# Performance work log

Measured on AMD Instinct MI355X. Metric: run time of the kernel, lower is better.

Reference implementation:

```python
import jax, jax.numpy as jnp
import numpy as np

MASK_RATIO = 0.02
N2V_W, WAV_W, TV_W = 1.0, 0.2, 0.01
THRESHOLD = 50.0
LEVELS = 3


def setup_inputs() -> dict:
    key = jax.random.key(0)
    k1, k2, k3 = jax.random.split(key, 3)
    shape = (64, 1, 512, 512)
    pred = jax.random.uniform(k1, shape, dtype=jnp.float32)
    noisy_input = jax.random.uniform(k2, shape, dtype=jnp.float32)
    # N2V random blind-spot mask (torch.rand_like(pred) < mask_ratio)
    mask = jax.random.uniform(k3, shape, dtype=jnp.float32) < MASK_RATIO
    return {"pred": pred, "noisy_input": noisy_input, "mask": mask}


def haar_dwt2(x):
    # x: [B, H, W] with H, W even. Single-level 2D Haar DWT (pywt 'haar').
    a = x[:, 0::2, 0::2]
    b = x[:, 0::2, 1::2]
    c = x[:, 1::2, 0::2]
    d = x[:, 1::2, 1::2]
    ll = (a + b + c + d) * 0.5
    ch = (a + b - c - d) * 0.5  # horizontal detail
    cv = (a - b + c - d) * 0.5  # vertical detail
    cd = (a - b - c + d) * 0.5  # diagonal detail
    return ll, ch, cv, cd


def _level_l1(c, thr):
    # L1 between coeff and its (detached) soft-thresholded version
    target = jax.lax.stop_gradient(jnp.sign(c) * jnp.maximum(jnp.abs(c) - thr, 0.0))
    return jnp.mean(jnp.abs(c - target))


def reference(pred, noisy_input, mask):
    p = jnp.clip(pred, 0.0, 1.0)

    # --- Noise2Void masked L1 ---
    m = mask.astype(p.dtype)
    n2v = jnp.sum(jnp.abs(p - noisy_input) * m) / jnp.maximum(jnp.sum(m), 1.0)

    # --- Wavelet sparsity (multi-level Haar, soft-threshold targets) ---
    x = p[:, 0]  # [B, H, W]
    details = []  # finest first
    for _ in range(LEVELS):
        x, ch, cv, cd = haar_dwt2(x)
        details.append((ch, cv, cd))
    wav = jnp.asarray(0.0, dtype=p.dtype)
    for level_idx in range(1, LEVELS + 1):  # level_idx=1 -> coarsest (wavedec2 order)
        ch, cv, cd = details[LEVELS - level_idx]
        thr = (THRESHOLD / (2.0 ** (level_idx - 1))) / 255.0
        lvl = (_level_l1(ch, thr) + _level_l1(cv, thr) + _level_l1(cd, thr)) / 3.0
        wav = wav + (1.0 / level_idx) * lvl

    # --- Total variation ---
    tv = jnp.mean(jnp.abs(p[:, :, 1:, :] - p[:, :, :-1, :])) + \
         jnp.mean(jnp.abs(p[:, :, :, 1:] - p[:, :, :, :-1]))

    return N2V_W * n2v + WAV_W * wav + TV_W * tv
```

## Files before the change

kernel.cpp:

```cpp
#include <hip/hip_runtime.h>

#define NIMG 64
#define H 512
#define W 512

constexpr float THR_64  = 50.0f / 255.0f;
constexpr float THR_128 = 50.0f / 2.0f / 255.0f;
constexpr float THR_256 = 50.0f / 4.0f / 255.0f;

__device__ __forceinline__ float wave_sum(float v) {
#pragma unroll
    for (int o = 32; o > 0; o >>= 1) v += __shfl_down(v, o, 64);
    return v;
}

__device__ __forceinline__ float clip01(float x) {
    return fminf(fmaxf(x, 0.0f), 1.0f);
}

__device__ __forceinline__ float4 clip4(float4 p) {
    p.x = clip01(p.x); p.y = clip01(p.y); p.z = clip01(p.z); p.w = clip01(p.w);
    return p;
}

__global__ __launch_bounds__(256) void kA(const float* __restrict__ pred,
                                          const float* __restrict__ noisy,
                                          const int* __restrict__ mask,
                                          float4* __restrict__ pA,
                                          float* __restrict__ pW2,
                                          float* __restrict__ ll2) {
    __shared__ float sl[9 * 512];
    __shared__ float red[4][5];

    const int tid = threadIdx.x;
    const int lane = tid & 63;
    const int wv = tid >> 6;
    const int bid = blockIdx.x;
    const int n = bid >> 6;
    const int s = bid & 63;
    const int r0 = s << 3;
    const size_t base = (size_t)n * (H * W) + (size_t)r0 * W;
    const size_t o0 = base + (size_t)tid * 4;

    float4 p0 = *reinterpret_cast<const float4*>(pred + o0);
    float4 p1 = *reinterpret_cast<const float4*>(pred + o0 + 1024);
    float4 p2 = *reinterpret_cast<const float4*>(pred + o0 + 2048);
    float4 p3 = *reinterpret_cast<const float4*>(pred + o0 + 3072);
    int4 m0 = *reinterpret_cast<const int4*>(mask + o0);
    int4 m1 = *reinterpret_cast<const int4*>(mask + o0 + 1024);
    int4 m2 = *reinterpret_cast<const int4*>(mask + o0 + 2048);
    int4 m3 = *reinterpret_cast<const int4*>(mask + o0 + 3072);
    if (tid < 128) {
        float4 hp = make_float4(0.f, 0.f, 0.f, 0.f);
        if (r0 > 0) {
            hp = clip4(*reinterpret_cast<const float4*>(pred + base - W + (size_t)tid * 4));
        }
        *reinterpret_cast<float4*>(&sl[(8 << 9) + (tid << 2)]) = hp;
    }

    float n2v = 0.0f, msum = 0.0f;
#define CHUNK(P, MK, OFS)                                                        \
    {                                                                            \
        float4 nz = make_float4(0.f, 0.f, 0.f, 0.f);                             \
        if ((MK.x | MK.y | MK.z | MK.w) != 0)                                    \
            nz = *reinterpret_cast<const float4*>(noisy + (OFS));                \
        P = clip4(P);                                                            \
        float m;                                                                 \
        m = MK.x ? 1.f : 0.f; n2v += fabsf(P.x - nz.x) * m; msum += m;           \
        m = MK.y ? 1.f : 0.f; n2v += fabsf(P.y - nz.y) * m; msum += m;           \
        m = MK.z ? 1.f : 0.f; n2v += fabsf(P.z - nz.z) * m; msum += m;           \
        m = MK.w ? 1.f : 0.f; n2v += fabsf(P.w - nz.w) * m; msum += m;           \
    }
    CHUNK(p0, m0, o0)
    CHUNK(p1, m1, o0 + 1024)
    CHUNK(p2, m2, o0 + 2048)
    CHUNK(p3, m3, o0 + 3072)
#undef CHUNK
    *reinterpret_cast<float4*>(&sl[tid << 2]) = p0;
    *reinterpret_cast<float4*>(&sl[(tid + 256) << 2]) = p1;
    *reinterpret_cast<float4*>(&sl[(tid + 512) << 2]) = p2;
    *reinterpret_cast<float4*>(&sl[(tid + 768) << 2]) = p3;
    __syncthreads();

    const int q2 = wv >> 1;
    const int h = wv & 1;
    const int cofs = (h << 8) + (lane << 2);
    const float* rowp = sl + (q2 << 11);

    float4 q0 = *reinterpret_cast<const float4*>(rowp + cofs);
    float4 q1 = *reinterpret_cast<const float4*>(rowp + 512 + cofs);
    float4 qq2 = *reinterpret_cast<const float4*>(rowp + 1024 + cofs);
    float4 q3 = *reinterpret_cast<const float4*>(rowp + 1536 + cofs);
    const float* hrow = (q2 == 1) ? (sl + 3 * 512) : (sl + 8 * 512);
    float4 hl = *reinterpret_cast<const float4*>(hrow + cofs);
    const bool has_halo = (q2 == 1) || (r0 > 0);

    float tv = 0.0f;
    tv += fabsf(q0.y - q0.x) + fabsf(q0.z - q0.y) + fabsf(q0.w - q0.z);
    tv += fabsf(q1.y - q1.x) + fabsf(q1.z - q1.y) + fabsf(q1.w - q1.z);
    tv += fabsf(qq2.y - qq2.x) + fabsf(qq2.z - qq2.y) + fabsf(qq2.w - qq2.z);
    tv += fabsf(q3.y - q3.x) + fabsf(q3.z - q3.y) + fabsf(q3.w - q3.z);
    float nx0 = __shfl_down(q0.x, 1, 64);
    float nx1 = __shfl_down(q1.x, 1, 64);
    float nx2 = __shfl_down(qq2.x, 1, 64);
    float nx3 = __shfl_down(q3.x, 1, 64);
    if (lane < 63) {
        tv += fabsf(nx0 - q0.w) + fabsf(nx1 - q1.w)
            + fabsf(nx2 - qq2.w) + fabsf(nx3 - q3.w);
    } else if (h == 0) {
        tv += fabsf(rowp[256] - q0.w) + fabsf(rowp[512 + 256] - q1.w)
            + fabsf(rowp[1024 + 256] - qq2.w) + fabsf(rowp[1536 + 256] - q3.w);
    }
    tv += fabsf(q1.x - q0.x) + fabsf(q1.y - q0.y) + fabsf(q1.z - q0.z) + fabsf(q1.w - q0.w);
    tv += fabsf(qq2.x - q1.x) + fabsf(qq2.y - q1.y) + fabsf(qq2.z - q1.z) + fabsf(qq2.w - q1.w);
    tv += fabsf(q3.x - qq2.x) + fabsf(q3.y - qq2.y) + fabsf(q3.z - qq2.z) + fabsf(q3.w - qq2.w);
    if (has_halo) {
        tv += fabsf(q0.x - hl.x) + fabsf(q0.y - hl.y)
            + fabsf(q0.z - hl.z) + fabsf(q0.w - hl.w);
    }

    float wav1 = 0.0f;
    float a, b, c, d, ch, cv, cd;
    a = q0.x; b = q0.y; c = q1.x; d = q1.y;
    float llA0 = (a + b + c + d) * 0.5f;
    ch = (a + b - c - d) * 0.5f; cv = (a - b + c - d) * 0.5f; cd = (a - b - c + d) * 0.5f;
    wav1 += fminf(fabsf(ch), THR_256) + fminf(fabsf(cv), THR_256) + fminf(fabsf(cd), THR_256);
    a = q0.z; b = q0.w; c = q1.z; d = q1.w;
    float llA1 = (a + b + c + d) * 0.5f;
    ch = (a + b - c - d) * 0.5f; cv = (a - b + c - d) * 0.5f; cd = (a - b - c + d) * 0.5f;
    wav1 += fminf(fabsf(ch), THR_256) + fminf(fabsf(cv), THR_256) + fminf(fabsf(cd), THR_256);
    a = qq2.x; b = qq2.y; c = q3.x; d = q3.y;
    float llB0 = (a + b + c + d) * 0.5f;
    ch = (a + b - c - d) * 0.5f; cv = (a - b + c - d) * 0.5f; cd = (a - b - c + d) * 0.5f;
    wav1 += fminf(fabsf(ch), THR_256) + fminf(fabsf(cv), THR_256) + fminf(fabsf(cd), THR_256);
    a = qq2.z; b = qq2.w; c = q3.z; d = q3.w;
    float llB1 = (a + b + c + d) * 0.5f;
    ch = (a + b - c - d) * 0.5f; cv = (a - b + c - d) * 0.5f; cd = (a - b - c + d) * 0.5f;
    wav1 += fminf(fabsf(ch), THR_256) + fminf(fabsf(cv), THR_256) + fminf(fabsf(cd), THR_256);

    float wav2, ll2v;
    {
        a = llA0; b = llA1; c = llB0; d = llB1;
        ll2v = (a + b + c + d) * 0.5f;
        ch = (a + b - c - d) * 0.5f;
        cv = (a - b + c - d) * 0.5f;
        cd = (a - b - c + d) * 0.5f;
        wav2 = fminf(fabsf(ch), THR_128) + fminf(fabsf(cv), THR_128) + fminf(fabsf(cd), THR_128);
    }
    ll2[(size_t)n * 16384 + (size_t)((s << 1) + q2) * 128 + (h << 6) + lane] = ll2v;

    float v0 = wave_sum(n2v);
    float v1 = wave_sum(msum);
    float v2 = wave_sum(tv);
    float v3 = wave_sum(wav1);
    float v4 = wave_sum(wav2);
    if (lane == 0) {
        red[wv][0] = v0; red[wv][1] = v1; red[wv][2] = v2;
        red[wv][3] = v3; red[wv][4] = v4;
    }
    __syncthreads();
    if (tid == 0) {
        pA[bid] = make_float4(red[0][0] + red[1][0] + red[2][0] + red[3][0],
                              red[0][1] + red[1][1] + red[2][1] + red[3][1],
                              red[0][2] + red[1][2] + red[2][2] + red[3][2],
                              red[0][3] + red[1][3] + red[2][3] + red[3][3]);
        pW2[bid] = red[0][4] + red[1][4] + red[2][4] + red[3][4];
    }
}

__global__ __launch_bounds__(256) void kC(const float* __restrict__ ll2,
                                          float* __restrict__ pC) {
    __shared__ float red[4];
    const int tid = threadIdx.x;
    const int lane = tid & 63, wv = tid >> 6;
    const int bid = blockIdx.x;
    const int n = bid >> 1;
    const int s = bid & 1;
    const float* src = ll2 + (size_t)n * 16384;

    float wav3 = 0.0f;
#pragma unroll
    for (int i = 0; i < 8; ++i) {
        int u = (i << 8) + tid;
        int qr = (s << 5) + (u >> 6);
        int qc = u & 63;
        float2 top = *reinterpret_cast<const float2*>(src + (2 * qr) * 128 + 2 * qc);
        float2 bot = *reinterpret_cast<const float2*>(src + (2 * qr + 1) * 128 + 2 * qc);
        float a = top.x, b = top.y, c = bot.x, d = bot.y;
        float ch = (a + b - c - d) * 0.5f;
        float cv = (a - b + c - d) * 0.5f;
        float cd = (a - b - c + d) * 0.5f;
        wav3 += fminf(fabsf(ch), THR_64) + fminf(fabsf(cv), THR_64) + fminf(fabsf(cd), THR_64);
    }
    float v = wave_sum(wav3);
    if (lane == 0) red[wv] = v;
    __syncthreads();
    if (tid == 0) pC[bid] = red[0] + red[1] + red[2] + red[3];
}

__global__ __launch_bounds__(256) void kD(const float4* __restrict__ pA,
                                          const float* __restrict__ pW2,
                                          const float* __restrict__ pC,
                                          float* __restrict__ out) {
    __shared__ float red[4][6];
    const int tid = threadIdx.x;
    const int lane = tid & 63, wv = tid >> 6;

    float s0 = 0, s1 = 0, s2 = 0, s3 = 0, s4 = 0, s5 = 0;
#pragma unroll
    for (int j = 0; j < 16; ++j) {
        float4 v = pA[tid + (j << 8)];
        s0 += v.x; s1 += v.y; s2 += v.z; s3 += v.w;
        s4 += pW2[tid + (j << 8)];
    }
    if (tid < 128) s5 = pC[tid];

    s0 = wave_sum(s0); s1 = wave_sum(s1); s2 = wave_sum(s2);
    s3 = wave_sum(s3); s4 = wave_sum(s4); s5 = wave_sum(s5);
    if (lane == 0) {
        red[wv][0] = s0; red[wv][1] = s1; red[wv][2] = s2;
        red[wv][3] = s3; red[wv][4] = s4; red[wv][5] = s5;
    }
    __syncthreads();
    if (tid == 0) {
        float a0 = red[0][0] + red[1][0] + red[2][0] + red[3][0];
        float a1 = red[0][1] + red[1][1] + red[2][1] + red[3][1];
        float a2 = red[0][2] + red[1][2] + red[2][2] + red[3][2];
        float a3 = red[0][3] + red[1][3] + red[2][3] + red[3][3];
        float a4 = red[0][4] + red[1][4] + red[2][4] + red[3][4];
        float a5 = red[0][5] + red[1][5] + red[2][5] + red[3][5];
        float n2v = a0 / fmaxf(a1, 1.0f);
        float tv = a2 / 16744448.0f;
        float wav = a3 * (1.0f / 37748736.0f)
                  + a4 * (1.0f / 6291456.0f)
                  + a5 * (1.0f / 786432.0f);
        out[0] = 1.0f * n2v + 0.2f * wav + 0.01f * tv;
    }
}

extern "C" void kernel_launch(void* const* d_in, const int* in_sizes, int n_in,
                              void* d_out, int out_size, void* d_ws, size_t ws_size,
                              hipStream_t stream) {
    (void)in_sizes; (void)n_in; (void)out_size; (void)ws_size;
    const float* pred  = (const float*)d_in[0];
    const float* noisy = (const float*)d_in[1];
    const int*   mask  = (const int*)d_in[2];

    float4* pA  = (float4*)d_ws;
    float*  pW2 = (float*)((char*)d_ws + 65536);
    float*  pC  = (float*)((char*)d_ws + 81920);
    float*  ll2 = (float*)((char*)d_ws + 98304);

    kA<<<4096, 256, 0, stream>>>(pred, noisy, mask, pA, pW2, ll2);
    kC<<<128, 256, 0, stream>>>(ll2, pC);
    kD<<<1, 256, 0, stream>>>(pA, pW2, pC, (float*)d_out);
}
```

Before: 192.5 us.

## Fuse third Haar level into main kernel and hoist noisy loads

Each block's 8 input rows give exactly a 2x128 tile of level-2 approximation coefficients, so level 3 is now computed in shared memory inside kA. This removes the kC kernel launch and the global ll2 write and read. The wavelet and TV partials are pre-scaled and merged into one accumulator, which cuts the number of wave reductions and shrinks the final reduction. The conditional noisy loads are also hoisted ahead of the arithmetic so they can be in flight together. The cost is an extra __syncthreads, and folding differently scaled terms into one float sum may change rounding slightly.

```diff
diff --git a/kernel.cpp b/kernel.cpp
--- a/kernel.cpp
+++ b/kernel.cpp
@@ -7,6 +7,11 @@
 constexpr float THR_64  = 50.0f / 255.0f;
 constexpr float THR_128 = 50.0f / 2.0f / 255.0f;
 constexpr float THR_256 = 50.0f / 4.0f / 255.0f;
+
+constexpr float SC_W1 = 0.2f  / 37748736.0f;
+constexpr float SC_W2 = 0.2f  / 6291456.0f;
+constexpr float SC_W3 = 0.2f  / 786432.0f;
+constexpr float SC_TV = 0.01f / 16744448.0f;
 
 __device__ __forceinline__ float wave_sum(float v) {
 #pragma unroll
@@ -26,11 +31,10 @@
 __global__ __launch_bounds__(256) void kA(const float* __restrict__ pred,
                                           const float* __restrict__ noisy,
                                           const int* __restrict__ mask,
-                                          float4* __restrict__ pA,
-                                          float* __restrict__ pW2,
-                                          float* __restrict__ ll2) {
+                                          float4* __restrict__ pA) {
     __shared__ float sl[9 * 512];
-    __shared__ float red[4][5];
+    __shared__ float sll2[2][128];
+    __shared__ float red[4][3];
 
     const int tid = threadIdx.x;
     const int lane = tid & 63;
@@ -58,24 +62,33 @@
         *reinterpret_cast<float4*>(&sl[(8 << 9) + (tid << 2)]) = hp;
     }
 
+    const bool b0 = (m0.x | m0.y | m0.z | m0.w) != 0;
+    const bool b1 = (m1.x | m1.y | m1.z | m1.w) != 0;
+    const bool b2 = (m2.x | m2.y | m2.z | m2.w) != 0;
+    const bool b3 = (m3.x | m3.y | m3.z | m3.w) != 0;
+    float4 nz0 = make_float4(0.f, 0.f, 0.f, 0.f);
+    float4 nz1 = nz0, nz2 = nz0, nz3 = nz0;
+    if (b0) nz0 = *reinterpret_cast<const float4*>(noisy + o0);
+    if (b1) nz1 = *reinterpret_cast<const float4*>(noisy + o0 + 1024);
+    if (b2) nz2 = *reinterpret_cast<const float4*>(noisy + o0 + 2048);
+    if (b3) nz3 = *reinterpret_cast<const float4*>(noisy + o0 + 3072);
+
+    p0 = clip4(p0); p1 = clip4(p1); p2 = clip4(p2); p3 = clip4(p3);
+
     float n2v = 0.0f, msum = 0.0f;
-#define CHUNK(P, MK, OFS)                                                        \
+#define ACC(P, MK, NZ)                                                           \
     {                                                                            \
-        float4 nz = make_float4(0.f, 0.f, 0.f, 0.f);                             \
-        if ((MK.x | MK.y | MK.z | MK.w) != 0)                                    \
-            nz = *reinterpret_cast<const float4*>(noisy + (OFS));                \
-        P = clip4(P);                                                            \
         float m;                                                                 \
-        m = MK.x ? 1.f : 0.f; n2v += fabsf(P.x - nz.x) * m; msum += m;           \
-        m = MK.y ? 1.f : 0.f; n2v += fabsf(P.y - nz.y) * m; msum += m;           \
-        m = MK.z ? 1.f : 0.f; n2v += fabsf(P.z - nz.z) * m; msum += m;           \
-        m = MK.w ? 1.f : 0.f; n2v += fabsf(P.w - nz.w) * m; msum += m;           \
-    }
-    CHUNK(p0, m0, o0)
-    CHUNK(p1, m1, o0 + 1024)
-    CHUNK(p2, m2, o0 + 2048)
-    CHUNK(p3, m3, o0 + 3072)
-#undef CHUNK
+        m = MK.x ? 1.f : 0.f; n2v += fabsf(P.x - NZ.x) * m; msum += m;           \
+        m = MK.y ? 1.f : 0.f; n2v += fabsf(P.y - NZ.y) * m; msum += m;           \
+        m = MK.z ? 1.f : 0.f; n2v += fabsf(P.z - NZ.z) * m; msum += m;           \
+        m = MK.w ? 1.f : 0.f; n2v += fabsf(P.w - NZ.w) * m; msum += m;           \
+    }
+    ACC(p0, m0, nz0)
+    ACC(p1, m1, nz1)
+    ACC(p2, m2, nz2)
+    ACC(p3, m3, nz3)
+#undef ACC
     *reinterpret_cast<float4*>(&sl[tid << 2]) = p0;
     *reinterpret_cast<float4*>(&sl[(tid + 256) << 2]) = p1;
     *reinterpret_cast<float4*>(&sl[(tid + 512) << 2]) = p2;
@@ -147,94 +160,59 @@
         cd = (a - b - c + d) * 0.5f;
         wav2 = fminf(fabsf(ch), THR_128) + fminf(fabsf(cv), THR_128) + fminf(fabsf(cd), THR_128);
     }
-    ll2[(size_t)n * 16384 + (size_t)((s << 1) + q2) * 128 + (h << 6) + lane] = ll2v;
+    sll2[q2][(h << 6) + lane] = ll2v;
+
+    float comb = wav1 * SC_W1 + wav2 * SC_W2 + tv * SC_TV;
+    __syncthreads();
+
+    if (wv == 0) {
+        float2 top = *reinterpret_cast<const float2*>(&sll2[0][lane << 1]);
+        float2 bot = *reinterpret_cast<const float2*>(&sll2[1][lane << 1]);
+        a = top.x; b = top.y; c = bot.x; d = bot.y;
+        ch = (a + b - c - d) * 0.5f;
+        cv = (a - b + c - d) * 0.5f;
+        cd = (a - b - c + d) * 0.5f;
+        comb += (fminf(fabsf(ch), THR_64) + fminf(fabsf(cv), THR_64)
+               + fminf(fabsf(cd), THR_64)) * SC_W3;
+    }
 
     float v0 = wave_sum(n2v);
     float v1 = wave_sum(msum);
-    float v2 = wave_sum(tv);
-    float v3 = wave_sum(wav1);
-    float v4 = wave_sum(wav2);
+    float v2 = wave_sum(comb);
     if (lane == 0) {
         red[wv][0] = v0; red[wv][1] = v1; red[wv][2] = v2;
-        red[wv][3] = v3; red[wv][4] = v4;
     }
     __syncthreads();
     if (tid == 0) {
         pA[bid] = make_float4(red[0][0] + red[1][0] + red[2][0] + red[3][0],
                               red[0][1] + red[1][1] + red[2][1] + red[3][1],
                               red[0][2] + red[1][2] + red[2][2] + red[3][2],
-                              red[0][3] + red[1][3] + red[2][3] + red[3][3]);
-        pW2[bid] = red[0][4] + red[1][4] + red[2][4] + red[3][4];
-    }
-}
-
-__global__ __launch_bounds__(256) void kC(const float* __restrict__ ll2,
-                                          float* __restrict__ pC) {
-    __shared__ float red[4];
+                              0.0f);
+    }
+}
+
+__global__ __launch_bounds__(256) void kD(const float4* __restrict__ pA,
+                                          float* __restrict__ out) {
+    __shared__ float red[4][3];
     const int tid = threadIdx.x;
     const int lane = tid & 63, wv = tid >> 6;
-    const int bid = blockIdx.x;
-    const int n = bid >> 1;
-    const int s = bid & 1;
-    const float* src = ll2 + (size_t)n * 16384;
-
-    float wav3 = 0.0f;
-#pragma unroll
-    for (int i = 0; i < 8; ++i) {
-        int u = (i << 8) + tid;
-        int qr = (s << 5) + (u >> 6);
-        int qc = u & 63;
-        float2 top = *reinterpret_cast<const float2*>(src + (2 * qr) * 128 + 2 * qc);
-        float2 bot = *reinterpret_cast<const float2*>(src + (2 * qr + 1) * 128 + 2 * qc);
-        float a = top.x, b = top.y, c = bot.x, d = bot.y;
-        float ch = (a + b - c - d) * 0.5f;
-        float cv = (a - b + c - d) * 0.5f;
-        float cd = (a - b - c + d) * 0.5f;
-        wav3 += fminf(fabsf(ch), THR_64) + fminf(fabsf(cv), THR_64) + fminf(fabsf(cd), THR_64);
-    }
-    float v = wave_sum(wav3);
-    if (lane == 0) red[wv] = v;
-    __syncthreads();
-    if (tid == 0) pC[bid] = red[0] + red[1] + red[2] + red[3];
-}
-
-__global__ __launch_bounds__(256) void kD(const float4* __restrict__ pA,
-                                          const float* __restrict__ pW2,
-                                          const float* __restrict__ pC,
-                                          float* __restrict__ out) {
-    __shared__ float red[4][6];
-    const int tid = threadIdx.x;
-    const int lane = tid & 63, wv = tid >> 6;
-
-    float s0 = 0, s1 = 0, s2 = 0, s3 = 0, s4 = 0, s5 = 0;
+
+    float s0 = 0, s1 = 0, s2 = 0;
 #pragma unroll
     for (int j = 0; j < 16; ++j) {
         float4 v = pA[tid + (j << 8)];
-        s0 += v.x; s1 += v.y; s2 += v.z; s3 += v.w;
-        s4 += pW2[tid + (j << 8)];
-    }
-    if (tid < 128) s5 = pC[tid];
-
+        s0 += v.x; s1 += v.y; s2 += v.z;
+    }
     s0 = wave_sum(s0); s1 = wave_sum(s1); s2 = wave_sum(s2);
-    s3 = wave_sum(s3); s4 = wave_sum(s4); s5 = wave_sum(s5);
     if (lane == 0) {
         red[wv][0] = s0; red[wv][1] = s1; red[wv][2] = s2;
-        red[wv][3] = s3; red[wv][4] = s4; red[wv][5] = s5;
     }
     __syncthreads();
     if (tid == 0) {
         float a0 = red[0][0] + red[1][0] + red[2][0] + red[3][0];
         float a1 = red[0][1] + red[1][1] + red[2][1] + red[3][1];
         float a2 = red[0][2] + red[1][2] + red[2][2] + red[3][2];
-        float a3 = red[0][3] + red[1][3] + red[2][3] + red[3][3];
-        float a4 = red[0][4] + red[1][4] + red[2][4] + red[3][4];
-        float a5 = red[0][5] + red[1][5] + red[2][5] + red[3][5];
-        float n2v = a0 / fmaxf(a1, 1.0f);
-        float tv = a2 / 16744448.0f;
-        float wav = a3 * (1.0f / 37748736.0f)
-                  + a4 * (1.0f / 6291456.0f)
-                  + a5 * (1.0f / 786432.0f);
-        out[0] = 1.0f * n2v + 0.2f * wav + 0.01f * tv;
+        out[0] = a0 / fmaxf(a1, 1.0f) + a2;
     }
 }
 
@@ -246,12 +224,8 @@
     const float* noisy = (const float*)d_in[1];
     const int*   mask  = (const int*)d_in[2];
 
-    float4* pA  = (float4*)d_ws;
-    float*  pW2 = (float*)((char*)d_ws + 65536);
-    float*  pC  = (float*)((char*)d_ws + 81920);
-    float*  ll2 = (float*)((char*)d_ws + 98304);
-
-    kA<<<4096, 256, 0, stream>>>(pred, noisy, mask, pA, pW2, ll2);
-    kC<<<128, 256, 0, stream>>>(ll2, pC);
-    kD<<<1, 256, 0, stream>>>(pA, pW2, pC, (float*)d_out);
-}
+    float4* pA = (float4*)d_ws;
+
+    kA<<<4096, 256, 0, stream>>>(pred, noisy, mask, pA);
+    kD<<<1, 256, 0, stream>>>(pA, (float*)d_out);
+}
```

New measurement: 189.4 us. About the same (-1.6%).
